# Performance work log

Hardware: AMD Instinct MI355X
Metric: run time of the kernel (lower is better)

The kernel has to match this reference:

```python
import jax, jax.numpy as jnp
import numpy as np

N, IN_DIM, OUT_DIM, H = 50000, 128, 128, 4
C = OUT_DIM // H  # 32, per-head channels
E = 1_600_000
NEG_SLOPE = 0.2
LN_EPS = 1e-5


def setup_inputs() -> dict:
    key = jax.random.key(0)
    ks = jax.random.split(key, 12)
    x = jax.random.normal(ks[0], (N, IN_DIM), dtype=jnp.float32)
    edge_index = jax.random.randint(ks[1], (2, E), 0, N, dtype=jnp.int64)
    edge_weight = jax.random.uniform(ks[2], (E,), dtype=jnp.float32)
    s = 1.0 / np.sqrt(IN_DIM)
    W = jax.random.normal(ks[3], (IN_DIM, H * C), dtype=jnp.float32) * s
    att_src = jax.random.normal(ks[4], (1, H, C), dtype=jnp.float32) * s
    att_dst = jax.random.normal(ks[5], (1, H, C), dtype=jnp.float32) * s
    W_edge = jax.random.normal(ks[6], (1, H * C), dtype=jnp.float32)
    att_edge = jax.random.normal(ks[7], (1, H, C), dtype=jnp.float32) * s
    bias = jnp.zeros((H * C,), dtype=jnp.float32)
    ln_gamma = jnp.ones((OUT_DIM,), dtype=jnp.float32)
    ln_beta = jnp.zeros((OUT_DIM,), dtype=jnp.float32)
    return {"x": x, "edge_index": edge_index, "edge_weight": edge_weight,
            "W": W, "att_src": att_src, "att_dst": att_dst,
            "W_edge": W_edge, "att_edge": att_edge, "bias": bias,
            "ln_gamma": ln_gamma, "ln_beta": ln_beta}


def _gat_forward(x, edge_index, edge_weight, W, att_src, att_dst, W_edge, att_edge, bias):
    # GATConv(in, C, heads=H, edge_dim=1), concat=True, add_self_loops=True (fill_value='mean')
    xp = (x @ W).reshape(N, H, C)                      # [N,H,C]
    a_src = jnp.sum(xp * att_src, axis=-1)             # [N,H]
    a_dst = jnp.sum(xp * att_dst, axis=-1)             # [N,H]

    # add self-loops; self-loop edge_attr = mean of existing edge_attr
    loop = jnp.arange(N, dtype=edge_index.dtype)
    src = jnp.concatenate([edge_index[0], loop])       # [E+N]
    dst = jnp.concatenate([edge_index[1], loop])
    ew = jnp.concatenate([edge_weight, jnp.full((N,), jnp.mean(edge_weight), edge_weight.dtype)])

    ea = (ew[:, None] @ W_edge).reshape(-1, H, C)      # [E+N,H,C]
    a_edge = jnp.sum(ea * att_edge, axis=-1)           # [E+N,H]

    logits = a_src[src] + a_dst[dst] + a_edge          # [E+N,H]
    logits = jax.nn.leaky_relu(logits, NEG_SLOPE)

    # segment softmax over destination-node neighborhoods
    m = jax.ops.segment_max(logits, dst, num_segments=N)     # [N,H]
    ex = jnp.exp(logits - m[dst])
    denom = jax.ops.segment_sum(ex, dst, num_segments=N)     # [N,H]
    attn = ex / (denom[dst] + 1e-16)                          # [E+N,H]

    msg = attn[:, :, None] * xp[src]                          # [E+N,H,C]
    out = jax.ops.segment_sum(msg, dst, num_segments=N)      # [N,H,C]
    return out.reshape(N, H * C) + bias


def reference(x, edge_index, edge_weight, W, att_src, att_dst, W_edge, att_edge, bias, ln_gamma, ln_beta):
    out = _gat_forward(x, edge_index, edge_weight, W, att_src, att_dst, W_edge, att_edge, bias)
    # LayerNorm
    mu = jnp.mean(out, axis=-1, keepdims=True)
    var = jnp.mean(jnp.square(out - mu), axis=-1, keepdims=True)
    out = (out - mu) / jnp.sqrt(var + LN_EPS) * ln_gamma + ln_beta
    # ELU (dropout is identity in eval)
    return jax.nn.elu(out)
```

## Files before the change

### kernel.cpp

```cpp
#include <hip/hip_runtime.h>
#include <hip/hip_fp16.h>
#include <cstddef>

#define N_NODES 50000
#define E_EDGES 1600000
#define NEG_SLOPE 0.2f
#define LN_EPS 1e-5f
#define LOG2E 1.4426950408889634f
#define PAD 96

#define NBK 782
#define BCAP 2560
#define PCH 4096
#define NCH 391
#define NGB 1563
#define TPB 256

#define OFF_SCAL    0u
#define OFF_BCUR    256u
#define OFF_EWPART  4096u
#define OFF_COUNTS  8192u
#define OFF_ASRC    208256u
#define OFF_ADST    1008256u
#define OFF_XPH     1808256u
#define OFF_PAIRS   14608256u
#define OFF_STAGE   33808256u

__device__ __forceinline__ float lrelu(float x) { return x > 0.f ? x : NEG_SLOPE * x; }

__device__ __forceinline__ float sel4(float4 v, int h) {
    float ab = (h & 1) ? v.y : v.x;
    float cd = (h & 1) ? v.w : v.z;
    return (h & 2) ? cd : ab;
}

__device__ __forceinline__ float4 fma4(float s, float4 a, float4 c) {
    c.x = fmaf(s, a.x, c.x); c.y = fmaf(s, a.y, c.y);
    c.z = fmaf(s, a.z, c.z); c.w = fmaf(s, a.w, c.w);
    return c;
}

__global__ __launch_bounds__(256, 5) void k_A(const float* __restrict__ x, const float* __restrict__ W,
                                              const float* __restrict__ att_src, const float* __restrict__ att_dst,
                                              const float* __restrict__ W_edge, const float* __restrict__ att_edge,
                                              const int* __restrict__ ei, const float* __restrict__ ew,
                                              unsigned short* __restrict__ xph, float* __restrict__ a_src,
                                              float* __restrict__ a_dst, float* __restrict__ scal,
                                              int* __restrict__ bcur, uint2* __restrict__ staging,
                                              float* __restrict__ ewPart) {
    __shared__ float sx[32 * 128];
    __shared__ float sW[32 * 128];
    int t = threadIdx.x;

    if (blockIdx.x < NCH) {
        int* cnt   = (int*)sx;
        int* gbase = cnt + NBK;
        float* wred = (float*)(gbase + NBK);
        for (int i = t; i < NBK; i += 256) cnt[i] = 0;
        __syncthreads();

        int e0 = blockIdx.x * PCH;
        int lr[16];
        float s_ew = 0.f;
        #pragma unroll
        for (int i = 0; i < 16; i++) {
            int e = e0 + i * 256 + t;
            lr[i] = 0;
            if (e < E_EDGES) {
                int d = ei[E_EDGES + e];
                s_ew += ew[e];
                lr[i] = atomicAdd(&cnt[d >> 6], 1);
            }
        }
        #pragma unroll
        for (int off = 32; off; off >>= 1) s_ew += __shfl_down(s_ew, off, 64);
        if ((t & 63) == 0) wred[t >> 6] = s_ew;
        __syncthreads();
        if (t == 0) ewPart[blockIdx.x] = wred[0] + wred[1] + wred[2] + wred[3];
        for (int i = t; i < NBK; i += 256) gbase[i] = atomicAdd(&bcur[i], cnt[i]);
        __syncthreads();

        #pragma unroll
        for (int i = 0; i < 16; i++) {
            int e = e0 + i * 256 + t;
            if (e < E_EDGES) {
                int s = ei[e];
                int d = ei[E_EDGES + e];
                float w = ew[e];
                int b = d >> 6;
                uint2 ent;
                ent.x = (unsigned int)s |
                        ((unsigned int)__half_as_ushort(__float2half_rn(w)) << 16);
                ent.y = (unsigned int)d;
                staging[(size_t)b * BCAP + gbase[b] + lr[i]] = ent;
            }
        }
        return;
    }

    int gb = blockIdx.x - NCH;
    if (gb == 0 && t < 128) {
        float p = W_edge[t] * att_edge[t];
        #pragma unroll
        for (int off = 16; off; off >>= 1) p += __shfl_down(p, off, 32);
        if ((t & 31) == 0) scal[4 + (t >> 5)] = p;
    }
    int r0 = gb * 32;
    int tc = t & 31;
    int tr = t >> 5;

    for (int i = t; i < 1024; i += 256) {
        int row = i >> 5;
        float4 v = make_float4(0.f, 0.f, 0.f, 0.f);
        if (r0 + row < N_NODES) v = ((const float4*)x)[(size_t)(r0 + row) * 32 + (i & 31)];
        ((float4*)sx)[i] = v;
    }

    float4 acc[4];
    #pragma unroll
    for (int r = 0; r < 4; r++) acc[r] = make_float4(0.f, 0.f, 0.f, 0.f);

    for (int kc = 0; kc < 128; kc += 32) {
        __syncthreads();
        for (int i = t; i < 1024; i += 256)
            ((float4*)sW)[i] = ((const float4*)W)[(size_t)kc * 32 + i];
        __syncthreads();
        #pragma unroll 4
        for (int k4 = 0; k4 < 8; k4++) {
            float4 w0 = ((float4*)sW)[(k4 * 4 + 0) * 32 + tc];
            float4 w1 = ((float4*)sW)[(k4 * 4 + 1) * 32 + tc];
            float4 w2 = ((float4*)sW)[(k4 * 4 + 2) * 32 + tc];
            float4 w3 = ((float4*)sW)[(k4 * 4 + 3) * 32 + tc];
            #pragma unroll
            for (int r = 0; r < 4; r++) {
                float4 xv = ((float4*)sx)[(tr * 4 + r) * 32 + (kc >> 2) + k4];
                acc[r] = fma4(xv.x, w0, acc[r]);
                acc[r] = fma4(xv.y, w1, acc[r]);
                acc[r] = fma4(xv.z, w2, acc[r]);
                acc[r] = fma4(xv.w, w3, acc[r]);
            }
        }
    }

    float4 s4 = ((const float4*)att_src)[tc];
    float4 d4 = ((const float4*)att_dst)[tc];
    int h = tc >> 3;
    #pragma unroll
    for (int r = 0; r < 4; r++) {
        int row = r0 + tr * 4 + r;
        if (row < N_NODES) {
            __half2 h01 = __floats2half2_rn(acc[r].x, acc[r].y);
            __half2 h23 = __floats2half2_rn(acc[r].z, acc[r].w);
            uint2 pk;
            pk.x = *(unsigned int*)&h01;
            pk.y = *(unsigned int*)&h23;
            ((uint2*)xph)[(size_t)row * 32 + tc] = pk;
            float ps = acc[r].x * s4.x + acc[r].y * s4.y + acc[r].z * s4.z + acc[r].w * s4.w;
            float pd = acc[r].x * d4.x + acc[r].y * d4.y + acc[r].z * d4.z + acc[r].w * d4.w;
            ps += __shfl_down(ps, 4, 8); ps += __shfl_down(ps, 2, 8); ps += __shfl_down(ps, 1, 8);
            pd += __shfl_down(pd, 4, 8); pd += __shfl_down(pd, 2, 8); pd += __shfl_down(pd, 1, 8);
            if ((tc & 7) == 0) {
                a_src[(size_t)row * 4 + h] = ps;
                a_dst[(size_t)row * 4 + h] = pd;
            }
        }
    }
}

__global__ __launch_bounds__(256) void k_p2(const uint2* __restrict__ staging,
                                            const int* __restrict__ bcur,
                                            const float* __restrict__ ewPart,
                                            unsigned int* __restrict__ pairs,
                                            int* __restrict__ counts, float* __restrict__ scal) {
    int b = blockIdx.x, t = threadIdx.x;
    __shared__ int cnt2[64];
    __shared__ float wr2[4];
    if (b == 0) {
        float s = 0.f;
        for (int i = t; i < NCH; i += 256) s += ewPart[i];
        #pragma unroll
        for (int off = 32; off; off >>= 1) s += __shfl_down(s, off, 64);
        if ((t & 63) == 0) wr2[t >> 6] = s;
    }
    if (t < 64) cnt2[t] = 0;
    __syncthreads();
    if (b == 0 && t == 0) scal[0] = wr2[0] + wr2[1] + wr2[2] + wr2[3];
    int tot = bcur[b];
    const uint2* sg = staging + (size_t)b * BCAP;
    for (int i = t; i < tot; i += 256) {
        uint2 ent = sg[i];
        int d = (int)ent.y;
        int r = atomicAdd(&cnt2[d & 63], 1);
        pairs[(size_t)d * PAD + r] = ent.x;
    }
    __syncthreads();
    int n = (b << 6) + t;
    if (t < 64 && n < N_NODES) counts[n] = cnt2[t];
}

__global__ __launch_bounds__(256) void k_p3(const unsigned int* __restrict__ xpu,
                                            const float* __restrict__ a_src,
                                            const float* __restrict__ a_dst,
                                            const int* __restrict__ counts,
                                            const unsigned int* __restrict__ pairs,
                                            const float* __restrict__ scal,
                                            const float* __restrict__ bias,
                                            const float* __restrict__ gamma,
                                            const float* __restrict__ beta,
                                            float* __restrict__ out) {
    __shared__ unsigned long long sal[4][4][100];
    int lane = threadIdx.x & 63;
    int wv = threadIdx.x >> 6;
    int n = blockIdx.x * 4 + wv;
    if (n >= N_NODES) return;

    int h = lane >> 4;
    int em = lane & 15;

    float4 K = *(const float4*)(scal + 4);
    float Kh = sel4(K, h);
    float mean_ew = scal[0] * (1.0f / E_EDGES);

    int cnt = __builtin_amdgcn_readfirstlane(counts[n]);
    float4 ad4 = *(const float4*)(a_dst + (size_t)4 * n);
    float4 as4 = *(const float4*)(a_src + (size_t)4 * n);
    float adh = sel4(ad4, h);
    float aself = exp2f(lrelu(sel4(as4, h) + adh + Kh * mean_ew) * LOG2E);

    unsigned int pv = xpu[(size_t)n * 64 + lane];
    float2 f = __half22float2(*(__half2*)&pv);
    float acc0 = aself * f.x, acc1 = aself * f.y;

    unsigned long long* sl = &sal[wv][h][0];
    const unsigned int* prow = pairs + (size_t)n * PAD;
    float den = 0.f;
    #pragma unroll
    for (int b = 0; b < 6; b++) {
        if (b * 16 < cnt) {
            int e = b * 16 + em;
            float alpha = 0.f;
            int s = n;
            if (e < cnt) {
                unsigned int pk = prow[e];
                s = (int)(pk & 0xFFFFu);
                float w = __half2float(__ushort_as_half((unsigned short)(pk >> 16)));
                float4 av = *(const float4*)(a_src + (size_t)4 * s);
                alpha = exp2f(lrelu(sel4(av, h) + adh + Kh * w) * LOG2E);
            }
            den += alpha;
            sl[e] = ((unsigned long long)__float_as_uint(alpha) << 32) | (unsigned int)s;
        }
    }

    int cnt4 = (cnt + 3) & ~3;
    for (int e = 0; e < cnt4; e += 4) {
        ulonglong2 p01 = *(const ulonglong2*)(sl + e);
        ulonglong2 p23 = *(const ulonglong2*)(sl + e + 2);
        unsigned long long pq[4] = {p01.x, p01.y, p23.x, p23.y};
        #pragma unroll
        for (int q = 0; q < 4; q++) {
            unsigned int sj = (unsigned int)pq[q];
            float aj = __uint_as_float((unsigned int)(pq[q] >> 32));
            unsigned int g = xpu[(size_t)sj * 64 + lane];
            __half2 hh = *(__half2*)&g;
            acc0 = fmaf(aj, __half2float(__low2half(hh)), acc0);
            acc1 = fmaf(aj, __half2float(__high2half(hh)), acc1);
        }
    }

    den += __shfl_xor(den, 1, 64);
    den += __shfl_xor(den, 2, 64);
    den += __shfl_xor(den, 4, 64);
    den += __shfl_xor(den, 8, 64);
    den += aself;

    float inv = 1.0f / (den + 1e-16f);
    float2 b2 = ((const float2*)bias)[lane];
    float y0 = fmaf(acc0, inv, b2.x);
    float y1 = fmaf(acc1, inv, b2.y);

    float s1 = y0 + y1;
    #pragma unroll
    for (int off = 1; off < 64; off <<= 1) s1 += __shfl_xor(s1, off, 64);
    float mu = s1 * (1.f / 128.f);
    float d0 = y0 - mu, d1 = y1 - mu;
    float s2 = d0 * d0 + d1 * d1;
    #pragma unroll
    for (int off = 1; off < 64; off <<= 1) s2 += __shfl_xor(s2, off, 64);
    float rstd = rsqrtf(s2 * (1.f / 128.f) + LN_EPS);
    float2 g2 = ((const float2*)gamma)[lane];
    float2 be2 = ((const float2*)beta)[lane];
    float o0 = fmaf(d0 * rstd, g2.x, be2.x);
    float o1 = fmaf(d1 * rstd, g2.y, be2.y);
    o0 = o0 > 0.f ? o0 : expm1f(o0);
    o1 = o1 > 0.f ? o1 : expm1f(o1);
    float2 o; o.x = o0; o.y = o1;
    ((float2*)out)[(size_t)n * 64 + lane] = o;
}

extern "C" void kernel_launch(void* const* d_in, const int* in_sizes, int n_in,
                              void* d_out, int out_size, void* d_ws, size_t ws_size,
                              hipStream_t stream) {
    const float* x        = (const float*)d_in[0];
    const int*   ei       = (const int*)d_in[1];
    const float* ew       = (const float*)d_in[2];
    const float* W        = (const float*)d_in[3];
    const float* att_src  = (const float*)d_in[4];
    const float* att_dst  = (const float*)d_in[5];
    const float* W_edge   = (const float*)d_in[6];
    const float* att_edge = (const float*)d_in[7];
    const float* bias     = (const float*)d_in[8];
    const float* gamma    = (const float*)d_in[9];
    const float* beta     = (const float*)d_in[10];
    float* out = (float*)d_out;

    char* ws = (char*)d_ws;
    float* scal      = (float*)(ws + OFF_SCAL);
    int*   bcur      = (int*)(ws + OFF_BCUR);
    float* ewPart    = (float*)(ws + OFF_EWPART);
    int*   counts    = (int*)(ws + OFF_COUNTS);
    float* a_src     = (float*)(ws + OFF_ASRC);
    float* a_dst     = (float*)(ws + OFF_ADST);
    unsigned short* xph = (unsigned short*)(ws + OFF_XPH);
    unsigned int* pairs = (unsigned int*)(ws + OFF_PAIRS);
    uint2* staging   = (uint2*)(ws + OFF_STAGE);

    hipMemsetAsync(bcur, 0, NBK * sizeof(int), stream);
    k_A<<<NCH + NGB, TPB, 0, stream>>>(x, W, att_src, att_dst, W_edge, att_edge, ei, ew,
                                       xph, a_src, a_dst, scal, bcur, staging, ewPart);
    k_p2<<<NBK, TPB, 0, stream>>>(staging, bcur, ewPart, pairs, counts, scal);
    k_p3<<<12500, TPB, 0, stream>>>((const unsigned int*)xph, a_src, a_dst, counts, pairs, scal,
                                    bias, gamma, beta, out);
}
```

Before: 222.6 us.

## Compute node projection x@W with fp16 MFMA instead of scalar FP32 FMAs

The x@W projection in k_A is rewritten to convert x and a transposed W to fp16 in padded shared memory and use mfma_f32_16x16x32_f16 instructions, with each wave computing a 32x32 output tile. Results are staged through shared memory so the existing epilogue (fp16 packing and attention dot products) can still read them. This targets the FP32 FMA cost of the GEMM. In exchange it loses input precision by rounding to fp16, transposes all of W per block, and raises shared memory use, which lowers the occupancy hint from 5 to 3.

```diff
diff --git a/kernel.cpp b/kernel.cpp
--- a/kernel.cpp
+++ b/kernel.cpp
@@ -26,6 +26,12 @@
 #define OFF_PAIRS   14608256u
 #define OFF_STAGE   33808256u
 
+#define XROW_B   272
+#define SWT_OFF  8704
+
+typedef _Float16 half8 __attribute__((ext_vector_type(8)));
+typedef float f32x4_t __attribute__((ext_vector_type(4)));
+
 __device__ __forceinline__ float lrelu(float x) { return x > 0.f ? x : NEG_SLOPE * x; }
 
 __device__ __forceinline__ float sel4(float4 v, int h) {
@@ -34,13 +40,7 @@
     return (h & 2) ? cd : ab;
 }
 
-__device__ __forceinline__ float4 fma4(float s, float4 a, float4 c) {
-    c.x = fmaf(s, a.x, c.x); c.y = fmaf(s, a.y, c.y);
-    c.z = fmaf(s, a.z, c.z); c.w = fmaf(s, a.w, c.w);
-    return c;
-}
-
-__global__ __launch_bounds__(256, 5) void k_A(const float* __restrict__ x, const float* __restrict__ W,
+__global__ __launch_bounds__(256, 3) void k_A(const float* __restrict__ x, const float* __restrict__ W,
                                               const float* __restrict__ att_src, const float* __restrict__ att_dst,
                                               const float* __restrict__ W_edge, const float* __restrict__ att_edge,
                                               const int* __restrict__ ei, const float* __restrict__ ew,
@@ -48,12 +48,11 @@
                                               float* __restrict__ a_dst, float* __restrict__ scal,
                                               int* __restrict__ bcur, uint2* __restrict__ staging,
                                               float* __restrict__ ewPart) {
-    __shared__ float sx[32 * 128];
-    __shared__ float sW[32 * 128];
+    __shared__ __align__(16) char smem[43520];
     int t = threadIdx.x;
 
     if (blockIdx.x < NCH) {
-        int* cnt   = (int*)sx;
+        int* cnt   = (int*)smem;
         int* gbase = cnt + NBK;
         float* wred = (float*)(gbase + NBK);
         for (int i = t; i < NBK; i += 256) cnt[i] = 0;
@@ -106,42 +105,67 @@
         if ((t & 31) == 0) scal[4 + (t >> 5)] = p;
     }
     int r0 = gb * 32;
+
+    for (int i = t; i < 1024; i += 256) {
+        int row = i >> 5, c4 = i & 31;
+        float4 v = make_float4(0.f, 0.f, 0.f, 0.f);
+        if (r0 + row < N_NODES) v = ((const float4*)x)[(size_t)(r0 + row) * 32 + c4];
+        __half2 h01 = __floats2half2_rn(v.x, v.y);
+        __half2 h23 = __floats2half2_rn(v.z, v.w);
+        uint2 pk;
+        pk.x = *(unsigned int*)&h01;
+        pk.y = *(unsigned int*)&h23;
+        *(uint2*)(smem + XROW_B * row + 8 * c4) = pk;
+    }
+    {
+        unsigned short* wt = (unsigned short*)(smem + SWT_OFF);
+        for (int i = t; i < 4096; i += 256) {
+            int k = i >> 5, c4 = i & 31;
+            float4 v = ((const float4*)W)[k * 32 + c4];
+            wt[(4 * c4 + 0) * 136 + k] = __half_as_ushort(__float2half_rn(v.x));
+            wt[(4 * c4 + 1) * 136 + k] = __half_as_ushort(__float2half_rn(v.y));
+            wt[(4 * c4 + 2) * 136 + k] = __half_as_ushort(__float2half_rn(v.z));
+            wt[(4 * c4 + 3) * 136 + k] = __half_as_ushort(__float2half_rn(v.w));
+        }
+    }
+    __syncthreads();
+
+    int lane = t & 63;
+    int wv = t >> 6;
+    int g = lane >> 4, q = lane & 15;
+    f32x4_t acc2[2][2] = {};
+    {
+        const char* pA = smem;
+        const char* pB = smem + SWT_OFF;
+        int cb = 32 * wv;
+        #pragma unroll
+        for (int s = 0; s < 4; s++) {
+            half8 a0 = *(const half8*)(pA + XROW_B * q + 64 * s + 16 * g);
+            half8 a1 = *(const half8*)(pA + XROW_B * (16 + q) + 64 * s + 16 * g);
+            half8 b0 = *(const half8*)(pB + XROW_B * (cb + q) + 64 * s + 16 * g);
+            half8 b1 = *(const half8*)(pB + XROW_B * (cb + 16 + q) + 64 * s + 16 * g);
+            acc2[0][0] = __builtin_amdgcn_mfma_f32_16x16x32_f16(a0, b0, acc2[0][0], 0, 0, 0);
+            acc2[0][1] = __builtin_amdgcn_mfma_f32_16x16x32_f16(a0, b1, acc2[0][1], 0, 0, 0);
+            acc2[1][0] = __builtin_amdgcn_mfma_f32_16x16x32_f16(a1, b0, acc2[1][0], 0, 0, 0);
+            acc2[1][1] = __builtin_amdgcn_mfma_f32_16x16x32_f16(a1, b1, acc2[1][1], 0, 0, 0);
+        }
+    }
+    __syncthreads();
+    float* sxp = (float*)smem;
+    {
+        int cb = 32 * wv;
+        #pragma unroll
+        for (int m = 0; m < 2; m++)
+            #pragma unroll
+            for (int nn = 0; nn < 2; nn++)
+                #pragma unroll
+                for (int r = 0; r < 4; r++)
+                    sxp[(m * 16 + g * 4 + r) * 128 + cb + nn * 16 + q] = acc2[m][nn][r];
+    }
+    __syncthreads();
+
     int tc = t & 31;
     int tr = t >> 5;
-
-    for (int i = t; i < 1024; i += 256) {
-        int row = i >> 5;
-        float4 v = make_float4(0.f, 0.f, 0.f, 0.f);
-        if (r0 + row < N_NODES) v = ((const float4*)x)[(size_t)(r0 + row) * 32 + (i & 31)];
-        ((float4*)sx)[i] = v;
-    }
-
-    float4 acc[4];
-    #pragma unroll
-    for (int r = 0; r < 4; r++) acc[r] = make_float4(0.f, 0.f, 0.f, 0.f);
-
-    for (int kc = 0; kc < 128; kc += 32) {
-        __syncthreads();
-        for (int i = t; i < 1024; i += 256)
-            ((float4*)sW)[i] = ((const float4*)W)[(size_t)kc * 32 + i];
-        __syncthreads();
-        #pragma unroll 4
-        for (int k4 = 0; k4 < 8; k4++) {
-            float4 w0 = ((float4*)sW)[(k4 * 4 + 0) * 32 + tc];
-            float4 w1 = ((float4*)sW)[(k4 * 4 + 1) * 32 + tc];
-            float4 w2 = ((float4*)sW)[(k4 * 4 + 2) * 32 + tc];
-            float4 w3 = ((float4*)sW)[(k4 * 4 + 3) * 32 + tc];
-            #pragma unroll
-            for (int r = 0; r < 4; r++) {
-                float4 xv = ((float4*)sx)[(tr * 4 + r) * 32 + (kc >> 2) + k4];
-                acc[r] = fma4(xv.x, w0, acc[r]);
-                acc[r] = fma4(xv.y, w1, acc[r]);
-                acc[r] = fma4(xv.z, w2, acc[r]);
-                acc[r] = fma4(xv.w, w3, acc[r]);
-            }
-        }
-    }
-
     float4 s4 = ((const float4*)att_src)[tc];
     float4 d4 = ((const float4*)att_dst)[tc];
     int h = tc >> 3;
@@ -149,14 +173,15 @@
     for (int r = 0; r < 4; r++) {
         int row = r0 + tr * 4 + r;
         if (row < N_NODES) {
-            __half2 h01 = __floats2half2_rn(acc[r].x, acc[r].y);
-            __half2 h23 = __floats2half2_rn(acc[r].z, acc[r].w);
+            float4 a = ((const float4*)sxp)[(tr * 4 + r) * 32 + tc];
+            __half2 h01 = __floats2half2_rn(a.x, a.y);
+            __half2 h23 = __floats2half2_rn(a.z, a.w);
             uint2 pk;
             pk.x = *(unsigned int*)&h01;
             pk.y = *(unsigned int*)&h23;
             ((uint2*)xph)[(size_t)row * 32 + tc] = pk;
-            float ps = acc[r].x * s4.x + acc[r].y * s4.y + acc[r].z * s4.z + acc[r].w * s4.w;
-            float pd = acc[r].x * d4.x + acc[r].y * d4.y + acc[r].z * d4.z + acc[r].w * d4.w;
+            float ps = a.x * s4.x + a.y * s4.y + a.z * s4.z + a.w * s4.w;
+            float pd = a.x * d4.x + a.y * d4.y + a.z * d4.z + a.w * d4.w;
             ps += __shfl_down(ps, 4, 8); ps += __shfl_down(ps, 2, 8); ps += __shfl_down(ps, 1, 8);
             pd += __shfl_down(pd, 4, 8); pd += __shfl_down(pd, 2, 8); pd += __shfl_down(pd, 1, 8);
             if ((tc & 7) == 0) {
```

Measured after the change: 227.1 us. 1.02x slower.
